# Kernel tuning notes

Hardware: AMD Instinct MI355X
Metric: run time of the kernel (lower is better)

## Reference

```python
import jax, jax.numpy as jnp
import numpy as np

NEG_INF = -1e9  # finite stand-in for -inf masked_fill (safe under softmax)


def setup_inputs() -> dict:
    B, T, S, D = 64, 128, 1024, 1024
    key = jax.random.key(0)
    k1, k2, k3, k4, k5, k6 = jax.random.split(key, 6)
    source = jax.random.normal(k1, (B, T, D), dtype=jnp.float32)
    memory_bank = jax.random.normal(k2, (B, S, D), dtype=jnp.float32)
    probs = jax.random.uniform(k3, (B, S), dtype=jnp.float32)
    # lengths in [S//2, S] so every row has valid positions
    memory_lengths = jax.random.randint(k4, (B,), S // 2, S + 1)
    scale = 1.0 / np.sqrt(D)
    W_in = jax.random.normal(k5, (D, D), dtype=jnp.float32) * scale   # linear_in.weight
    W_out = jax.random.normal(k6, (D, 2 * D), dtype=jnp.float32) * scale  # linear_out.weight (no bias)
    return {"source": source, "memory_bank": memory_bank, "probs": probs,
            "memory_lengths": memory_lengths, "W_in": W_in, "W_out": W_out}


def reference(source, memory_bank, probs, memory_lengths, W_in, W_out):
    B, T, D = source.shape
    S = memory_bank.shape[1]
    # score (general): (source @ W_in^T) @ memory_bank^T -> [B, T, S]
    q = jnp.einsum('btd,ed->bte', source, W_in)
    align = jnp.einsum('bte,bse->bts', q, memory_bank)
    # length mask [B, 1, S]
    mask = (jnp.arange(S)[None, :] < memory_lengths[:, None])[:, None, :]
    align = jnp.where(mask, align, NEG_INF)
    # softmax before rescale
    norescale_av = jax.nn.softmax(align, axis=-1)                 # [B, T, S]
    # rescale by key probabilities, re-mask, renormalize
    scaled = norescale_av * probs[:, None, :]
    scaled = scaled * mask.astype(scaled.dtype)
    align_vectors = scaled / jnp.sum(scaled, axis=-1, keepdims=True)
    # context
    c = jnp.einsum('bts,bsd->btd', align_vectors, memory_bank)    # [B, T, D]
    # concat + linear_out + tanh
    concat_c = jnp.concatenate([c, source], axis=-1)              # [B, T, 2D]
    attn_h = jnp.tanh(jnp.einsum('btf,df->btd', concat_c, W_out))
    # outputs are [tgt_len, batch, ...]
    return (attn_h.transpose(1, 0, 2),
            align_vectors.transpose(1, 0, 2),
            norescale_av.transpose(1, 0, 2))
```

## Files before the change

### kernel.cpp

```cpp
#include <hip/hip_runtime.h>
#include <cmath>

constexpr int Bn = 64;
constexpr int Tn = 128;
constexpr int Sn = 1024;
constexpr int Dn = 1024;

typedef __attribute__((ext_vector_type(8))) _Float16 half8;
typedef __attribute__((ext_vector_type(4))) _Float16 half4;
typedef __attribute__((ext_vector_type(4))) float float4v;

__device__ __forceinline__ void split2(float x, _Float16& h, _Float16& l) {
  h = (_Float16)x;
  l = (_Float16)(x - (float)h);
}

__global__ void __launch_bounds__(256) cvtw_k(const float* __restrict__ Win,
                                              const float* __restrict__ Wout,
                                              _Float16* __restrict__ winh,
                                              _Float16* __restrict__ winl,
                                              _Float16* __restrict__ wouth) {
  const int idx = blockIdx.x * 256 + threadIdx.x;
  const int nWin = (Dn * Dn) / 4;
  const int nWout = (Dn * 2 * Dn) / 4;
  if (idx < nWin) {
    const float4 v = reinterpret_cast<const float4*>(Win)[idx];
    _Float16 h0, h1, h2, h3, l0, l1, l2, l3;
    split2(v.x, h0, l0); split2(v.y, h1, l1); split2(v.z, h2, l2); split2(v.w, h3, l3);
    half4 hv = {h0, h1, h2, h3};
    half4 lv = {l0, l1, l2, l3};
    reinterpret_cast<half4*>(winh)[idx] = hv;
    reinterpret_cast<half4*>(winl)[idx] = lv;
  } else if (idx < nWin + nWout) {
    const int j = idx - nWin;
    const float4 v = reinterpret_cast<const float4*>(Wout)[j];
    half4 hv = {(_Float16)v.x, (_Float16)v.y, (_Float16)v.z, (_Float16)v.w};
    reinterpret_cast<half4*>(wouth)[j] = hv;
  }
}


__device__ __forceinline__ void stageT_split(const float* __restrict__ G, size_t ld,
                                             int row0, int k0,
                                             _Float16 (*Sh)[40], _Float16 (*Sl)[40],
                                             int tid) {
#pragma unroll
  for (int it = 0; it < 4; ++it) {
    const int f = tid + it * 256;
    const int r = f >> 3, kq = (f & 7) << 2;
    const float4 v = *reinterpret_cast<const float4*>(G + (size_t)(row0 + r) * ld + k0 + kq);
    _Float16 h0, h1, h2, h3, l0, l1, l2, l3;
    split2(v.x, h0, l0); split2(v.y, h1, l1); split2(v.z, h2, l2); split2(v.w, h3, l3);
    half4 hv = {h0, h1, h2, h3};
    half4 lv = {l0, l1, l2, l3};
    *reinterpret_cast<half4*>(&Sh[r][kq]) = hv;
    *reinterpret_cast<half4*>(&Sl[r][kq]) = lv;
  }
}

__device__ __forceinline__ void stageT_split64(const float* __restrict__ G, size_t ld,
                                               int row0, int k0,
                                               _Float16 (*Sh)[40], _Float16 (*Sl)[40],
                                               int tid) {
#pragma unroll
  for (int it = 0; it < 2; ++it) {
    const int f = tid + it * 256;
    const int r = f >> 3, kq = (f & 7) << 2;
    const float4 v = *reinterpret_cast<const float4*>(G + (size_t)(row0 + r) * ld + k0 + kq);
    _Float16 h0, h1, h2, h3, l0, l1, l2, l3;
    split2(v.x, h0, l0); split2(v.y, h1, l1); split2(v.z, h2, l2); split2(v.w, h3, l3);
    half4 hv = {h0, h1, h2, h3};
    half4 lv = {l0, l1, l2, l3};
    *reinterpret_cast<half4*>(&Sh[r][kq]) = hv;
    *reinterpret_cast<half4*>(&Sl[r][kq]) = lv;
  }
}

__device__ __forceinline__ void stageT_plain(const float* __restrict__ G, size_t ld,
                                             int row0, int k0,
                                             _Float16 (*Sh)[40], int tid) {
#pragma unroll
  for (int it = 0; it < 4; ++it) {
    const int f = tid + it * 256;
    const int r = f >> 3, kq = (f & 7) << 2;
    const float4 v = *reinterpret_cast<const float4*>(G + (size_t)(row0 + r) * ld + k0 + kq);
    half4 hv = {(_Float16)v.x, (_Float16)v.y, (_Float16)v.z, (_Float16)v.w};
    *reinterpret_cast<half4*>(&Sh[r][kq]) = hv;
  }
}

__device__ __forceinline__ void stageT_h16(const _Float16* __restrict__ Gh,
                                           const _Float16* __restrict__ Gl, size_t ld,
                                           int row0, int k0,
                                           _Float16 (*Sh)[40], _Float16 (*Sl)[40],
                                           int tid) {
#pragma unroll
  for (int it = 0; it < 2; ++it) {
    const int f = tid + it * 256;
    const int r = f >> 2, kq = (f & 3) << 3;
    *reinterpret_cast<half8*>(&Sh[r][kq]) =
        *reinterpret_cast<const half8*>(Gh + (size_t)(row0 + r) * ld + k0 + kq);
    *reinterpret_cast<half8*>(&Sl[r][kq]) =
        *reinterpret_cast<const half8*>(Gl + (size_t)(row0 + r) * ld + k0 + kq);
  }
}

__device__ __forceinline__ void stageB_trans(const float* __restrict__ G, size_t ld,
                                             int k0, int col0,
                                             _Float16 (*Bt)[44], int tid) {
  const int d = tid & 127;
  const int kb = (tid >> 7) * 4;
#pragma unroll
  for (int it = 0; it < 4; ++it) {
    const int kq = kb + it * 8;
    _Float16 h[4];
#pragma unroll
    for (int j = 0; j < 4; ++j)
      h[j] = (_Float16)G[(size_t)(k0 + kq + j) * ld + col0 + d];
    half4 hv = {h[0], h[1], h[2], h[3]};
    *reinterpret_cast<half4*>(&Bt[d][kq]) = hv;
  }
}


__device__ __forceinline__ void stage64x64_h16(const _Float16* __restrict__ G, size_t ld,
                                               int row0, int k0,
                                               _Float16 (*Sh)[72], int tid) {
#pragma unroll
  for (int it = 0; it < 2; ++it) {
    const int f = tid + it * 256;
    const int r = f >> 3, kq = (f & 7) << 3;
    *reinterpret_cast<half8*>(&Sh[r][kq]) =
        *reinterpret_cast<const half8*>(G + (size_t)(row0 + r) * ld + k0 + kq);
  }
}

__device__ __forceinline__ void stage64x64_f32(const float* __restrict__ G, size_t ld,
                                               int row0, int k0,
                                               _Float16 (*Sh)[72], int tid) {
#pragma unroll
  for (int it = 0; it < 4; ++it) {
    const int f = tid + it * 256;
    const int r = f >> 4, kq = (f & 15) << 2;
    const float4 v = *reinterpret_cast<const float4*>(G + (size_t)(row0 + r) * ld + k0 + kq);
    half4 hv = {(_Float16)v.x, (_Float16)v.y, (_Float16)v.z, (_Float16)v.w};
    *reinterpret_cast<half4*>(&Sh[r][kq]) = hv;
  }
}

__device__ __forceinline__ void stage128x64_h16(const _Float16* __restrict__ G, size_t ld,
                                                int row0, int k0,
                                                _Float16 (*Sh)[72], int tid) {
#pragma unroll
  for (int it = 0; it < 4; ++it) {
    const int f = tid + it * 256;
    const int r = f >> 3, kq = (f & 7) << 3;
    *reinterpret_cast<half8*>(&Sh[r][kq]) =
        *reinterpret_cast<const half8*>(G + (size_t)(row0 + r) * ld + k0 + kq);
  }
}


__device__ __forceinline__ void mma64_split3(const _Float16 (*Ah)[40], const _Float16 (*Al)[40],
                                             const _Float16 (*Bh)[40], const _Float16 (*Bl)[40],
                                             float4v acc[4][2], int lane, int wc) {
  const int g = lane >> 4, rr = lane & 15, kb = g << 3;
  half8 ah[4], al[4];
#pragma unroll
  for (int m = 0; m < 4; ++m) {
    ah[m] = *reinterpret_cast<const half8*>(&Ah[m * 16 + rr][kb]);
    al[m] = *reinterpret_cast<const half8*>(&Al[m * 16 + rr][kb]);
  }
#pragma unroll
  for (int n = 0; n < 2; ++n) {
    const half8 bh = *reinterpret_cast<const half8*>(&Bh[wc * 32 + n * 16 + rr][kb]);
    const half8 bl = *reinterpret_cast<const half8*>(&Bl[wc * 32 + n * 16 + rr][kb]);
#pragma unroll
    for (int m = 0; m < 4; ++m) {
      acc[m][n] = __builtin_amdgcn_mfma_f32_16x16x32_f16(ah[m], bh, acc[m][n], 0, 0, 0);
      acc[m][n] = __builtin_amdgcn_mfma_f32_16x16x32_f16(al[m], bh, acc[m][n], 0, 0, 0);
      acc[m][n] = __builtin_amdgcn_mfma_f32_16x16x32_f16(ah[m], bl, acc[m][n], 0, 0, 0);
    }
  }
}

__device__ __forceinline__ void mma128_split3(const _Float16 (*Ah)[40], const _Float16 (*Al)[40],
                                              const _Float16 (*Bh)[40], const _Float16 (*Bl)[40],
                                              float4v acc[4][4], int lane, int wr, int wc) {
  const int g = lane >> 4, rr = lane & 15, kb = g << 3;
  half8 ah[4], al[4];
#pragma unroll
  for (int m = 0; m < 4; ++m) {
    ah[m] = *reinterpret_cast<const half8*>(&Ah[wr * 64 + m * 16 + rr][kb]);
    al[m] = *reinterpret_cast<const half8*>(&Al[wr * 64 + m * 16 + rr][kb]);
  }
#pragma unroll
  for (int n = 0; n < 4; ++n) {
    const half8 bh = *reinterpret_cast<const half8*>(&Bh[wc * 64 + n * 16 + rr][kb]);
    const half8 bl = *reinterpret_cast<const half8*>(&Bl[wc * 64 + n * 16 + rr][kb]);
#pragma unroll
    for (int m = 0; m < 4; ++m) {
      acc[m][n] = __builtin_amdgcn_mfma_f32_16x16x32_f16(ah[m], bh, acc[m][n], 0, 0, 0);
      acc[m][n] = __builtin_amdgcn_mfma_f32_16x16x32_f16(al[m], bh, acc[m][n], 0, 0, 0);
      acc[m][n] = __builtin_amdgcn_mfma_f32_16x16x32_f16(ah[m], bl, acc[m][n], 0, 0, 0);
    }
  }
}

__device__ __forceinline__ void mma128_bt(const _Float16 (*Ah)[40], const _Float16 (*Bt)[44],
                                          float4v acc[4][4], int lane, int wr, int wc) {
  const int g = lane >> 4, rr = lane & 15, kb = g << 3;
  half8 ah[4];
#pragma unroll
  for (int m = 0; m < 4; ++m)
    ah[m] = *reinterpret_cast<const half8*>(&Ah[wr * 64 + m * 16 + rr][kb]);
#pragma unroll
  for (int n = 0; n < 4; ++n) {
    const half8 b = *reinterpret_cast<const half8*>(&Bt[wc * 64 + n * 16 + rr][kb]);
#pragma unroll
    for (int m = 0; m < 4; ++m)
      acc[m][n] = __builtin_amdgcn_mfma_f32_16x16x32_f16(ah[m], b, acc[m][n], 0, 0, 0);
  }
}

__device__ __forceinline__ void mma64_bk64_plain(const _Float16 (*Ah)[72], const _Float16 (*Bh)[72],
                                                 float4v acc[4][2], int lane, int wc) {
  const int g = lane >> 4, rr = lane & 15;
#pragma unroll
  for (int kk = 0; kk < 2; ++kk) {
    const int kb = kk * 32 + (g << 3);
    half8 ah[4];
#pragma unroll
    for (int m = 0; m < 4; ++m)
      ah[m] = *reinterpret_cast<const half8*>(&Ah[m * 16 + rr][kb]);
#pragma unroll
    for (int n = 0; n < 2; ++n) {
      const half8 b = *reinterpret_cast<const half8*>(&Bh[wc * 32 + n * 16 + rr][kb]);
#pragma unroll
      for (int m = 0; m < 4; ++m)
        acc[m][n] = __builtin_amdgcn_mfma_f32_16x16x32_f16(ah[m], b, acc[m][n], 0, 0, 0);
    }
  }
}

__global__ void __launch_bounds__(256) g1_k(const float* __restrict__ src,
                                            const _Float16* __restrict__ winh,
                                            const _Float16* __restrict__ winl,
                                            _Float16* __restrict__ qh,
                                            _Float16* __restrict__ ql) {
  __shared__ _Float16 Ah[64][40], Al[64][40], Bh[128][40], Bl[128][40];
  const int tid = threadIdx.x, lane = tid & 63, wc = tid >> 6;
  const int f = blockIdx.y * 8 + blockIdx.x;
  const int w = (f & 7) * 128 + (f >> 3);
  const int row0 = (w >> 3) * 64, col0 = (w & 7) * 128;
  float4v acc[4][2] = {};
  for (int k0 = 0; k0 < Dn; k0 += 32) {
    stageT_split64(src, Dn, row0, k0, Ah, Al, tid);
    stageT_h16(winh, winl, Dn, col0, k0, Bh, Bl, tid);
    __syncthreads();
    mma64_split3(Ah, Al, Bh, Bl, acc, lane, wc);
    __syncthreads();
  }
  const int g = lane >> 4, rr = lane & 15;
#pragma unroll
  for (int m = 0; m < 4; ++m)
#pragma unroll
    for (int n = 0; n < 2; ++n)
#pragma unroll
      for (int i = 0; i < 4; ++i) {
        const int row = row0 + m * 16 + g * 4 + i;
        const int col = col0 + wc * 32 + n * 16 + rr;
        _Float16 h, l; split2(acc[m][n][i], h, l);
        qh[(size_t)row * Dn + col] = h;
        ql[(size_t)row * Dn + col] = l;
      }
}

__global__ void __launch_bounds__(256) g2_k(const _Float16* __restrict__ qh,
                                            const _Float16* __restrict__ ql,
                                            const float* __restrict__ mb,
                                            const int* __restrict__ lens,
                                            float* __restrict__ out1) {
  __shared__ _Float16 Ah[128][40], Al[128][40], Bh[128][40], Bl[128][40];
  const int tid = threadIdx.x, lane = tid & 63, wv = tid >> 6;
  const int wr = wv >> 1, wc = wv & 1;
  const int id = blockIdx.z * 8 + blockIdx.x;
  const int j = id >> 3;
  const int b = (id & 7) * 8 + (j >> 3), col0 = (j & 7) * 128;
  if (col0 >= lens[b]) return;
  const _Float16* qhb = qh + (size_t)b * Tn * Dn;
  const _Float16* qlb = ql + (size_t)b * Tn * Dn;
  const float* mbb = mb + (size_t)b * Sn * Dn;
  float* Cb = out1 + (size_t)b * Sn;
  float4v acc[4][4] = {};
  for (int k0 = 0; k0 < Dn; k0 += 32) {
    stageT_h16(qhb, qlb, Dn, 0, k0, Ah, Al, tid);
    stageT_split(mbb, Dn, col0, k0, Bh, Bl, tid);
    __syncthreads();
    mma128_split3(Ah, Al, Bh, Bl, acc, lane, wr, wc);
    __syncthreads();
  }
  const int g = lane >> 4, rr = lane & 15;
#pragma unroll
  for (int m = 0; m < 4; ++m)
#pragma unroll
    for (int n = 0; n < 4; ++n)
#pragma unroll
      for (int i = 0; i < 4; ++i) {
        const int t = wr * 64 + m * 16 + g * 4 + i;
        const int s = col0 + wc * 64 + n * 16 + rr;
        Cb[(size_t)t * (Bn * Sn) + s] = acc[m][n][i];
      }
}

__device__ __forceinline__ float block_max(float v, float* red, int tid) {
#pragma unroll
  for (int o = 32; o; o >>= 1) v = fmaxf(v, __shfl_xor(v, o));
  if ((tid & 63) == 0) red[tid >> 6] = v;
  __syncthreads();
  v = fmaxf(fmaxf(red[0], red[1]), fmaxf(red[2], red[3]));
  __syncthreads();
  return v;
}

__device__ __forceinline__ float block_sum(float v, float* red, int tid) {
#pragma unroll
  for (int o = 32; o; o >>= 1) v += __shfl_xor(v, o);
  if ((tid & 63) == 0) red[tid >> 6] = v;
  __syncthreads();
  v = red[0] + red[1] + red[2] + red[3];
  __syncthreads();
  return v;
}

__global__ void __launch_bounds__(256) softmax_k(float* __restrict__ av_io,
                                                 const float* __restrict__ probs,
                                                 const int* __restrict__ lens,
                                                 float* __restrict__ out_nore) {
  __shared__ float red[4];
  const int r = blockIdx.x;
  const int b = r & (Bn - 1);
  const int tid = threadIdx.x;
  const int len = lens[b];
  float* row = av_io + (size_t)r * Sn;
  const int s0 = tid * 4;

  const float4 x = *reinterpret_cast<const float4*>(row + s0);
  const bool v0 = (s0 + 0) < len, v1 = (s0 + 1) < len, v2 = (s0 + 2) < len, v3 = (s0 + 3) < len;

  float lm = -1e30f;
  if (v0) lm = fmaxf(lm, x.x);
  if (v1) lm = fmaxf(lm, x.y);
  if (v2) lm = fmaxf(lm, x.z);
  if (v3) lm = fmaxf(lm, x.w);
  const float m = block_max(lm, red, tid);

  const float e0 = v0 ? __expf(x.x - m) : 0.f;
  const float e1 = v1 ? __expf(x.y - m) : 0.f;
  const float e2 = v2 ? __expf(x.z - m) : 0.f;
  const float e3 = v3 ? __expf(x.w - m) : 0.f;
  const float esum = block_sum(e0 + e1 + e2 + e3, red, tid);
  const float rs = 1.f / esum;
  const float n0 = e0 * rs, n1 = e1 * rs, n2 = e2 * rs, n3 = e3 * rs;
  *reinterpret_cast<float4*>(out_nore + (size_t)r * Sn + s0) = make_float4(n0, n1, n2, n3);

  const float4 p = *reinterpret_cast<const float4*>(probs + (size_t)b * Sn + s0);
  const float c0 = n0 * p.x, c1 = n1 * p.y, c2 = n2 * p.z, c3 = n3 * p.w;
  const float ssum = block_sum(c0 + c1 + c2 + c3, red, tid);
  const float rss = 1.f / ssum;
  const float a0 = c0 * rss, a1 = c1 * rss, a2 = c2 * rss, a3 = c3 * rss;
  *reinterpret_cast<float4*>(row + s0) = make_float4(a0, a1, a2, a3);
}

__global__ void __launch_bounds__(256) g4_k(const float* __restrict__ av,
                                            const float* __restrict__ mb,
                                            const int* __restrict__ lens,
                                            _Float16* __restrict__ c) {
  __shared__ _Float16 Ah[128][40];
  __shared__ _Float16 Bt[128][44];
  const int tid = threadIdx.x, lane = tid & 63, wv = tid >> 6;
  const int wr = wv >> 1, wc = wv & 1;
  const int id = blockIdx.z * 8 + blockIdx.x;
  const int j = id >> 3;
  const int b = (id & 7) * 8 + (j >> 3), col0 = (j & 7) * 128;
  const int kmax = (lens[b] + 31) & ~31;
  const float* avb = av + (size_t)b * Sn;
  const float* mbb = mb + (size_t)b * Sn * Dn;
  _Float16* cb = c + (size_t)b * Tn * Dn;
  float4v acc[4][4] = {};
  for (int k0 = 0; k0 < kmax; k0 += 32) {
    stageT_plain(avb, (size_t)Bn * Sn, 0, k0, Ah, tid);
    stageB_trans(mbb, Dn, k0, col0, Bt, tid);
    __syncthreads();
    mma128_bt(Ah, Bt, acc, lane, wr, wc);
    __syncthreads();
  }
  const int g = lane >> 4, rr = lane & 15;
#pragma unroll
  for (int m = 0; m < 4; ++m)
#pragma unroll
    for (int n = 0; n < 4; ++n)
#pragma unroll
      for (int i = 0; i < 4; ++i) {
        const int t = wr * 64 + m * 16 + g * 4 + i;
        const int d = col0 + wc * 64 + n * 16 + rr;
        cb[(size_t)t * Dn + d] = (_Float16)acc[m][n][i];
      }
}

__global__ void __launch_bounds__(256) g5_k(const _Float16* __restrict__ c,
                                            const float* __restrict__ src,
                                            const _Float16* __restrict__ wouth,
                                            float* __restrict__ out0) {
  __shared__ _Float16 Ah[64][72], Bh[128][72];
  const int tid = threadIdx.x, lane = tid & 63, wc = tid >> 6;
  const int f = blockIdx.y * 8 + blockIdx.x;
  const int w = (f & 7) * 128 + (f >> 3);
  const int row0 = (w >> 3) * 64, col0 = (w & 7) * 128;
  float4v acc[4][2] = {};
  for (int k0 = 0; k0 < 2 * Dn; k0 += 64) {
    if (k0 < Dn) stage64x64_h16(c, Dn, row0, k0, Ah, tid);
    else         stage64x64_f32(src, Dn, row0, k0 - Dn, Ah, tid);
    stage128x64_h16(wouth, 2 * Dn, col0, k0, Bh, tid);
    __syncthreads();
    mma64_bk64_plain(Ah, Bh, acc, lane, wc);
    __syncthreads();
  }
  const int g = lane >> 4, rr = lane & 15;
#pragma unroll
  for (int m = 0; m < 4; ++m)
#pragma unroll
    for (int n = 0; n < 2; ++n)
#pragma unroll
      for (int i = 0; i < 4; ++i) {
        const int mm = row0 + m * 16 + g * 4 + i;
        const int bb = mm >> 7;
        const int t = mm & 127;
        const int d = col0 + wc * 32 + n * 16 + rr;
        out0[((size_t)t * Bn + bb) * Dn + d] = tanhf(acc[m][n][i]);
      }
}


extern "C" void kernel_launch(void* const* d_in, const int* in_sizes, int n_in,
                              void* d_out, int out_size, void* d_ws, size_t ws_size,
                              hipStream_t stream) {
  const float* src   = (const float*)d_in[0];
  const float* mb    = (const float*)d_in[1];
  const float* probs = (const float*)d_in[2];
  const int*   lens  = (const int*)d_in[3];
  const float* Win   = (const float*)d_in[4];
  const float* Wout  = (const float*)d_in[5];

  float* out  = (float*)d_out;
  float* out0 = out;
  float* out1 = out + (size_t)Tn * Bn * Dn;
  float* out2 = out1 + (size_t)Tn * Bn * Sn;

  const size_t BTD = (size_t)Bn * Tn * Dn;
  _Float16* qh    = (_Float16*)d_ws;
  _Float16* ql    = qh + BTD;
  _Float16* winh  = ql + BTD;
  _Float16* winl  = winh + (size_t)Dn * Dn;
  _Float16* wouth = winl + (size_t)Dn * Dn;
  _Float16* cbuf  = (_Float16*)d_ws;

  cvtw_k<<<(Dn * Dn / 4 + Dn * 2 * Dn / 4 + 255) / 256, 256, 0, stream>>>(
      Win, Wout, winh, winl, wouth);

  g1_k<<<dim3(Dn / 128, (Bn * Tn) / 64), 256, 0, stream>>>(src, winh, winl, qh, ql);

  g2_k<<<dim3(8, 1, Bn), 256, 0, stream>>>(qh, ql, mb, lens, out1);

  softmax_k<<<Tn * Bn, 256, 0, stream>>>(out1, probs, lens, out2);

  g4_k<<<dim3(Dn / 128, 1, Bn), 256, 0, stream>>>(out1, mb, lens, cbuf);

  g5_k<<<dim3(Dn / 128, (Bn * Tn) / 64), 256, 0, stream>>>(cbuf, src, wouth, out0);
}
```

Measured before the change: 302.0 us.

## Enlarge output GEMM tile to 128x128 and coalesce q stores via LDS

The final linear_out GEMM moves from 64x128 tiles with one wave per 32 columns to 128x128 tiles with a 2x2 wave grid. This doubles the reuse of each staged weight tile and halves the grid size. Separately, the input-projection kernel now stages its hi/lo fp16 outputs through a shared LDS transpose buffer and writes them back as 16-byte vector stores instead of scattered 2-byte stores. The costs are more accumulator registers per thread and fewer blocks, which may lower occupancy.

Result: slower. 310.7 us (+2.9%).

```diff
diff --git a/kernel.cpp b/kernel.cpp
--- a/kernel.cpp
+++ b/kernel.cpp
@@ -122,12 +122,11 @@
   }
 }
 
-
-__device__ __forceinline__ void stage64x64_h16(const _Float16* __restrict__ G, size_t ld,
-                                               int row0, int k0,
-                                               _Float16 (*Sh)[72], int tid) {
-#pragma unroll
-  for (int it = 0; it < 2; ++it) {
+__device__ __forceinline__ void stage128x64_h16(const _Float16* __restrict__ G, size_t ld,
+                                                int row0, int k0,
+                                                _Float16 (*Sh)[72], int tid) {
+#pragma unroll
+  for (int it = 0; it < 4; ++it) {
     const int f = tid + it * 256;
     const int r = f >> 3, kq = (f & 7) << 3;
     *reinterpret_cast<half8*>(&Sh[r][kq]) =
@@ -135,28 +134,16 @@
   }
 }
 
-__device__ __forceinline__ void stage64x64_f32(const float* __restrict__ G, size_t ld,
-                                               int row0, int k0,
-                                               _Float16 (*Sh)[72], int tid) {
-#pragma unroll
-  for (int it = 0; it < 4; ++it) {
+__device__ __forceinline__ void stage128x64_f32(const float* __restrict__ G, size_t ld,
+                                                int row0, int k0,
+                                                _Float16 (*Sh)[72], int tid) {
+#pragma unroll
+  for (int it = 0; it < 8; ++it) {
     const int f = tid + it * 256;
     const int r = f >> 4, kq = (f & 15) << 2;
     const float4 v = *reinterpret_cast<const float4*>(G + (size_t)(row0 + r) * ld + k0 + kq);
     half4 hv = {(_Float16)v.x, (_Float16)v.y, (_Float16)v.z, (_Float16)v.w};
     *reinterpret_cast<half4*>(&Sh[r][kq]) = hv;
-  }
-}
-
-__device__ __forceinline__ void stage128x64_h16(const _Float16* __restrict__ G, size_t ld,
-                                                int row0, int k0,
-                                                _Float16 (*Sh)[72], int tid) {
-#pragma unroll
-  for (int it = 0; it < 4; ++it) {
-    const int f = tid + it * 256;
-    const int r = f >> 3, kq = (f & 7) << 3;
-    *reinterpret_cast<half8*>(&Sh[r][kq]) =
-        *reinterpret_cast<const half8*>(G + (size_t)(row0 + r) * ld + k0 + kq);
   }
 }
 
@@ -223,8 +210,8 @@
   }
 }
 
-__device__ __forceinline__ void mma64_bk64_plain(const _Float16 (*Ah)[72], const _Float16 (*Bh)[72],
-                                                 float4v acc[4][2], int lane, int wc) {
+__device__ __forceinline__ void mma128_bk64(const _Float16 (*Ah)[72], const _Float16 (*Bh)[72],
+                                            float4v acc[4][4], int lane, int wr, int wc) {
   const int g = lane >> 4, rr = lane & 15;
 #pragma unroll
   for (int kk = 0; kk < 2; ++kk) {
@@ -232,10 +219,10 @@
     half8 ah[4];
 #pragma unroll
     for (int m = 0; m < 4; ++m)
-      ah[m] = *reinterpret_cast<const half8*>(&Ah[m * 16 + rr][kb]);
-#pragma unroll
-    for (int n = 0; n < 2; ++n) {
-      const half8 b = *reinterpret_cast<const half8*>(&Bh[wc * 32 + n * 16 + rr][kb]);
+      ah[m] = *reinterpret_cast<const half8*>(&Ah[wr * 64 + m * 16 + rr][kb]);
+#pragma unroll
+    for (int n = 0; n < 4; ++n) {
+      const half8 b = *reinterpret_cast<const half8*>(&Bh[wc * 64 + n * 16 + rr][kb]);
 #pragma unroll
       for (int m = 0; m < 4; ++m)
         acc[m][n] = __builtin_amdgcn_mfma_f32_16x16x32_f16(ah[m], b, acc[m][n], 0, 0, 0);
@@ -248,7 +235,11 @@
                                             const _Float16* __restrict__ winl,
                                             _Float16* __restrict__ qh,
                                             _Float16* __restrict__ ql) {
-  __shared__ _Float16 Ah[64][40], Al[64][40], Bh[128][40], Bl[128][40];
+  __shared__ _Float16 lds[15360];
+  _Float16 (*Ah)[40] = (_Float16(*)[40])lds;
+  _Float16 (*Al)[40] = (_Float16(*)[40])(lds + 2560);
+  _Float16 (*Bh)[40] = (_Float16(*)[40])(lds + 5120);
+  _Float16 (*Bl)[40] = (_Float16(*)[40])(lds + 10240);
   const int tid = threadIdx.x, lane = tid & 63, wc = tid >> 6;
   const int f = blockIdx.y * 8 + blockIdx.x;
   const int w = (f & 7) * 128 + (f >> 3);
@@ -261,19 +252,30 @@
     mma64_split3(Ah, Al, Bh, Bl, acc, lane, wc);
     __syncthreads();
   }
+  _Float16 (*T)[136] = (_Float16(*)[136])lds;
   const int g = lane >> 4, rr = lane & 15;
 #pragma unroll
-  for (int m = 0; m < 4; ++m)
-#pragma unroll
-    for (int n = 0; n < 2; ++n)
-#pragma unroll
-      for (int i = 0; i < 4; ++i) {
-        const int row = row0 + m * 16 + g * 4 + i;
-        const int col = col0 + wc * 32 + n * 16 + rr;
-        _Float16 h, l; split2(acc[m][n][i], h, l);
-        qh[(size_t)row * Dn + col] = h;
-        ql[(size_t)row * Dn + col] = l;
-      }
+  for (int pass = 0; pass < 2; ++pass) {
+    __syncthreads();
+#pragma unroll
+    for (int m = 0; m < 4; ++m)
+#pragma unroll
+      for (int n = 0; n < 2; ++n)
+#pragma unroll
+        for (int i = 0; i < 4; ++i) {
+          _Float16 h, l; split2(acc[m][n][i], h, l);
+          T[m * 16 + g * 4 + i][wc * 32 + n * 16 + rr] = pass == 0 ? h : l;
+        }
+    __syncthreads();
+    _Float16* dst = pass == 0 ? qh : ql;
+#pragma unroll
+    for (int it = 0; it < 4; ++it) {
+      const int idx = tid + it * 256;
+      const int r = idx >> 4, c8 = (idx & 15) << 3;
+      *reinterpret_cast<half8*>(dst + (size_t)(row0 + r) * Dn + col0 + c8) =
+          *reinterpret_cast<const half8*>(&T[r][c8]);
+    }
+  }
 }
 
 __global__ void __launch_bounds__(256) g2_k(const _Float16* __restrict__ qh,
@@ -412,31 +414,32 @@
                                             const float* __restrict__ src,
                                             const _Float16* __restrict__ wouth,
                                             float* __restrict__ out0) {
-  __shared__ _Float16 Ah[64][72], Bh[128][72];
-  const int tid = threadIdx.x, lane = tid & 63, wc = tid >> 6;
+  __shared__ _Float16 Ah[128][72], Bh[128][72];
+  const int tid = threadIdx.x, lane = tid & 63, wv = tid >> 6;
+  const int wr = wv >> 1, wc = wv & 1;
   const int f = blockIdx.y * 8 + blockIdx.x;
-  const int w = (f & 7) * 128 + (f >> 3);
-  const int row0 = (w >> 3) * 64, col0 = (w & 7) * 128;
-  float4v acc[4][2] = {};
+  const int w = (f & 7) * 64 + (f >> 3);
+  const int row0 = (w >> 3) * 128, col0 = (w & 7) * 128;
+  float4v acc[4][4] = {};
   for (int k0 = 0; k0 < 2 * Dn; k0 += 64) {
-    if (k0 < Dn) stage64x64_h16(c, Dn, row0, k0, Ah, tid);
-    else         stage64x64_f32(src, Dn, row0, k0 - Dn, Ah, tid);
+    if (k0 < Dn) stage128x64_h16(c, Dn, row0, k0, Ah, tid);
+    else         stage128x64_f32(src, Dn, row0, k0 - Dn, Ah, tid);
     stage128x64_h16(wouth, 2 * Dn, col0, k0, Bh, tid);
     __syncthreads();
-    mma64_bk64_plain(Ah, Bh, acc, lane, wc);
+    mma128_bk64(Ah, Bh, acc, lane, wr, wc);
     __syncthreads();
   }
   const int g = lane >> 4, rr = lane & 15;
+  const int bb = row0 >> 7;
 #pragma unroll
   for (int m = 0; m < 4; ++m)
 #pragma unroll
-    for (int n = 0; n < 2; ++n)
+    for (int n = 0; n < 4; ++n)
 #pragma unroll
       for (int i = 0; i < 4; ++i) {
-        const int mm = row0 + m * 16 + g * 4 + i;
-        const int bb = mm >> 7;
+        const int mm = row0 + wr * 64 + m * 16 + g * 4 + i;
         const int t = mm & 127;
-        const int d = col0 + wc * 32 + n * 16 + rr;
+        const int d = col0 + wc * 64 + n * 16 + rr;
         out0[((size_t)t * Bn + bb) * Dn + d] = tanhf(acc[m][n][i]);
       }
 }
@@ -476,5 +479,5 @@
 
   g4_k<<<dim3(Dn / 128, 1, Bn), 256, 0, stream>>>(out1, mb, lens, cbuf);
 
-  g5_k<<<dim3(Dn / 128, (Bn * Tn) / 64), 256, 0, stream>>>(cbuf, src, wouth, out0);
-}
+  g5_k<<<dim3(8, 64), 256, 0, stream>>>(cbuf, src, wouth, out0);
+}
```
